# Optimization experiments

Measured on AMD Instinct MI355X. Metric: run time of the kernel, lower is better.

Reference implementation:

```python
import jax, jax.numpy as jnp
import numpy as np

STALENESS_LAMBDA = 0.001
TEMPERATURE = 1.0
TOP_K = 3
EPS = 1e-8


def setup_inputs() -> dict:
    key = jax.random.key(0)
    ks = jax.random.split(key, 6)
    B, D, H, E = 131072, 512, 256, 10
    features = jax.random.normal(ks[0], (B, D), dtype=jnp.float32)
    W_proj = jax.random.normal(ks[1], (D, H), dtype=jnp.float32) * 0.02
    b_proj = jnp.zeros((H,), dtype=jnp.float32)
    expert_emb = jax.random.normal(ks[2], (E, H), dtype=jnp.float32) * 0.01
    expert_features = jax.random.normal(ks[3], (E, D), dtype=jnp.float32)
    trust = jax.random.uniform(ks[4], (E,), dtype=jnp.float32)
    delta_t = jax.random.uniform(ks[5], (E,), dtype=jnp.float32) * 100.0
    return {"features": features, "W_proj": W_proj, "b_proj": b_proj,
            "expert_emb": expert_emb, "expert_features": expert_features,
            "trust": trust, "delta_t": delta_t}


def reference(features, W_proj, b_proj, expert_emb, expert_features, trust, delta_t):
    H = W_proj.shape[1]
    # learned gate: sigmoid(proj(x) . e_j / sqrt(H))  -> (B, E)
    proj = features @ W_proj + b_proj                                  # (B, H)
    gate = jax.nn.sigmoid(jnp.einsum('bh,eh->be', proj, expert_emb)
                          / jnp.sqrt(jnp.float32(H)))
    # cosine similarity S_ij mapped to [0, 1]                          # (B, E)
    fn = features / jnp.maximum(jnp.linalg.norm(features, axis=1, keepdims=True), EPS)
    en = expert_features / jnp.maximum(
        jnp.linalg.norm(expert_features, axis=1, keepdims=True), EPS)
    sim = (jnp.einsum('bd,ed->be', fn, en) + 1.0) * 0.5
    # staleness decay e^{-lambda * dt} and base score T*S*decay
    stale = jnp.exp(-STALENESS_LAMBDA * delta_t)                        # (E,)
    score = gate * (trust * stale)[None, :] * sim                       # (B, E)
    probs = jax.nn.softmax(score / TEMPERATURE, axis=-1)                # (B, E)
    topk_w, topk_idx = jax.lax.top_k(probs, TOP_K)                      # (B, K)
    topk_w = topk_w / jnp.sum(topk_w, axis=-1, keepdims=True)
    return topk_w, topk_idx, probs
```

## Files before the change

kernel.cpp:

```cpp
#include <hip/hip_runtime.h>
#include <stdint.h>
#include <math.h>

#define D_DIM 512
#define H_DIM 256
#define E_NUM 10

typedef float f16v __attribute__((ext_vector_type(16)));
typedef float f2 __attribute__((ext_vector_type(2)));

__global__ __launch_bounds__(256) void pre_wg(const float* __restrict__ Wp,
                                              const float* __restrict__ bp,
                                              const float* __restrict__ emb,
                                              float* __restrict__ pk,
                                              float* __restrict__ bg) {
  int gid = blockIdx.x * 256 + threadIdx.x;
  if (gid < E_NUM * D_DIM) {
    int d = gid / E_NUM;
    int e = gid - d * E_NUM;
    const float* wr = Wp + (size_t)d * H_DIM;
    const float* er = emb + (size_t)e * H_DIM;
    float s0 = 0.f, s1 = 0.f, s2 = 0.f, s3 = 0.f;
#pragma unroll 4
    for (int h = 0; h < H_DIM; h += 4) {
      float4 a = *(const float4*)(wr + h);
      float4 b = *(const float4*)(er + h);
      s0 = fmaf(a.x, b.x, s0); s1 = fmaf(a.y, b.y, s1);
      s2 = fmaf(a.z, b.z, s2); s3 = fmaf(a.w, b.w, s3);
    }
    pk[(size_t)d * 20 + e] = ((s0 + s1) + (s2 + s3)) * 0.0625f;
  } else if (gid < E_NUM * D_DIM + E_NUM) {
    int e = gid - E_NUM * D_DIM;
    const float* er = emb + (size_t)e * H_DIM;
    float s = 0.f;
    for (int h = 0; h < H_DIM; ++h) s = fmaf(bp[h], er[h], s);
    bg[e] = s * 0.0625f;
  }
}

__global__ __launch_bounds__(64) void pre_en(const float* __restrict__ ef,
                                             const float* __restrict__ trust,
                                             const float* __restrict__ dtv,
                                             float* __restrict__ pk,
                                             float* __restrict__ cf) {
  int e = blockIdx.x, l = threadIdx.x;
  const float* row = ef + (size_t)e * D_DIM;
  float s = 0.f;
#pragma unroll
  for (int j = 0; j < D_DIM / 64; ++j) { float v = row[l + 64 * j]; s = fmaf(v, v, s); }
#pragma unroll
  for (int o = 32; o; o >>= 1) s += __shfl_xor(s, o, 64);
  float inv = 1.f / fmaxf(sqrtf(s), 1e-8f);
#pragma unroll
  for (int j = 0; j < D_DIM / 64; ++j) {
    int d = l + 64 * j;
    pk[(size_t)d * 20 + 10 + e] = row[d] * inv;
  }
  if (l == 0) cf[e] = trust[e] * expf(-0.001f * dtv[e]);
}

#define WVx(i) ((i) < 16 ? w0[(i) & 15] : (i) < 32 ? w1[(i) & 15] : \
                (i) < 48 ? w2[(i) & 15] : (i) < 64 ? w3[(i) & 15] : w4[(i) & 15])

__global__ __launch_bounds__(256, 6) void router_main(
    const float* __restrict__ feat, const float* __restrict__ pk,
    const float* __restrict__ cf, const float* __restrict__ bg,
    float* __restrict__ out, int B) {
  __shared__ float red[3 * 64 * 23];
  const int t = threadIdx.x;
  const int l = t & 63;
  const int w = __builtin_amdgcn_readfirstlane(t >> 6);
  const size_t row = (size_t)blockIdx.x * 64 + l;
  const float* gp = feat + row * D_DIM + w * 128;
  const float* wq = pk + (size_t)w * 128 * 20;

  f2 ag[5], as_[5], n2;
#pragma unroll
  for (int i = 0; i < 5; ++i) { ag[i] = f2{0.f, 0.f}; as_[i] = f2{0.f, 0.f}; }
  n2 = f2{0.f, 0.f};

  float4 fvA[4], fvB[4];
#pragma unroll
  for (int j = 0; j < 4; ++j) fvA[j] = *(const float4*)(gp + j * 4);

#pragma unroll
  for (int it = 0; it < 8; ++it) {
    float4* cur = (it & 1) ? fvB : fvA;
    float4* nxt = (it & 1) ? fvA : fvB;
    if (it < 7) {
#pragma unroll
      for (int j = 0; j < 4; ++j) nxt[j] = *(const float4*)(gp + (it + 1) * 16 + j * 4);
    }
#pragma unroll
    for (int sub = 0; sub < 4; ++sub) {
      f16v w0, w1, w2, w3, w4;
      const float* wp = wq + (it * 4 + sub) * 80;
      asm volatile(
          "s_load_dwordx16 %0, %5, 0x0\n"
          "s_load_dwordx16 %1, %5, 0x40\n"
          "s_load_dwordx16 %2, %5, 0x80\n"
          "s_load_dwordx16 %3, %5, 0xc0\n"
          "s_load_dwordx16 %4, %5, 0x100\n"
          "s_waitcnt lgkmcnt(0)"
          : "=&s"(w0), "=&s"(w1), "=&s"(w2), "=&s"(w3), "=&s"(w4)
          : "s"(wp));
      float4 f = cur[sub];
#pragma unroll
      for (int q = 0; q < 4; ++q) {
        const float fq = (q == 0) ? f.x : (q == 1) ? f.y : (q == 2) ? f.z : f.w;
        const f2 fq2 = {fq, fq};
#pragma unroll
        for (int j = 0; j < 5; ++j) {
          const int bgi = q * 20 + 2 * j;
          f2 wg2 = {WVx(bgi), WVx(bgi + 1)};
          ag[j] = __builtin_elementwise_fma(fq2, wg2, ag[j]);
        }
#pragma unroll
        for (int j = 0; j < 5; ++j) {
          const int bsi = q * 20 + 10 + 2 * j;
          f2 ws2 = {WVx(bsi), WVx(bsi + 1)};
          as_[j] = __builtin_elementwise_fma(fq2, ws2, as_[j]);
        }
      }
      f2 p0 = {f.x, f.y}, p1 = {f.z, f.w};
      n2 = __builtin_elementwise_fma(p0, p0, n2);
      n2 = __builtin_elementwise_fma(p1, p1, n2);
    }
  }

  float acc[21];
#pragma unroll
  for (int e = 0; e < E_NUM; ++e) { acc[e] = ag[e >> 1][e & 1]; acc[10 + e] = as_[e >> 1][e & 1]; }
  acc[20] = n2.x + n2.y;

  if (w) {
    float* rp = &red[((w - 1) * 64 + l) * 23];
#pragma unroll
    for (int i = 0; i < 21; ++i) rp[i] = acc[i];
  }
  __syncthreads();
  if (w == 0) {
#pragma unroll
    for (int s = 0; s < 3; ++s) {
      const float* rp = &red[(s * 64 + l) * 23];
#pragma unroll
      for (int i = 0; i < 21; ++i) acc[i] += rp[i];
    }

    const float inv = 1.f / fmaxf(sqrtf(acc[20]), 1e-8f);
    float probs[E_NUM];
    float m = -1e30f;
#pragma unroll
    for (int e = 0; e < E_NUM; ++e) {
      float logit = acc[e] + bg[e];
      float gate = 1.f / (1.f + __expf(-logit));
      float sim = fmaf(acc[10 + e] * inv, 0.5f, 0.5f);
      float sc = gate * cf[e] * sim;
      probs[e] = sc;
      m = fmaxf(m, sc);
    }
    float Z = 0.f;
#pragma unroll
    for (int e = 0; e < E_NUM; ++e) { float pe = __expf(probs[e] - m); probs[e] = pe; Z += pe; }
    const float invZ = 1.f / Z;
#pragma unroll
    for (int e = 0; e < E_NUM; ++e) probs[e] *= invZ;

    int i0 = 0; float b0 = probs[0];
#pragma unroll
    for (int e = 1; e < E_NUM; ++e) if (probs[e] > b0) { b0 = probs[e]; i0 = e; }
    int i1 = -1; float b1 = -1.f;
#pragma unroll
    for (int e = 0; e < E_NUM; ++e) if (e != i0 && probs[e] > b1) { b1 = probs[e]; i1 = e; }
    int i2 = -1; float b2 = -1.f;
#pragma unroll
    for (int e = 0; e < E_NUM; ++e) if (e != i0 && e != i1 && probs[e] > b2) { b2 = probs[e]; i2 = e; }

    const float wnorm = 1.f / (b0 + b1 + b2);
    float* ow = out + row * 3;
    ow[0] = b0 * wnorm; ow[1] = b1 * wnorm; ow[2] = b2 * wnorm;
    float* oi = out + (size_t)B * 3 + row * 3;
    oi[0] = (float)i0; oi[1] = (float)i1; oi[2] = (float)i2;
    float* op = out + (size_t)B * 6 + row * E_NUM;
#pragma unroll
    for (int e = 0; e < E_NUM; ++e) op[e] = probs[e];
  }
}

extern "C" void kernel_launch(void* const* d_in, const int* in_sizes, int n_in,
                              void* d_out, int out_size, void* d_ws, size_t ws_size,
                              hipStream_t stream) {
  const float* feat  = (const float*)d_in[0];
  const float* Wp    = (const float*)d_in[1];
  const float* bp    = (const float*)d_in[2];
  const float* emb   = (const float*)d_in[3];
  const float* ef    = (const float*)d_in[4];
  const float* trust = (const float*)d_in[5];
  const float* dtv   = (const float*)d_in[6];
  float* out = (float*)d_out;

  float* pk = (float*)d_ws;
  float* cf = pk + D_DIM * 20;
  float* bg = cf + E_NUM;

  const int B = in_sizes[0] / D_DIM;

  hipLaunchKernelGGL(pre_wg, dim3((E_NUM * D_DIM + E_NUM + 255) / 256), dim3(256),
                     0, stream, Wp, bp, emb, pk, bg);
  hipLaunchKernelGGL(pre_en, dim3(E_NUM), dim3(64), 0, stream, ef, trust, dtv, pk, cf);
  hipLaunchKernelGGL(router_main, dim3(B / 64), dim3(256), 0, stream,
                     feat, pk, cf, bg, out, B);
}
```

Baseline: 73.68 us.

## Stage feature rows through LDS with async global_load_lds multi-buffer pipeline

Replaces direct per-thread register loads of feature rows with a 4-deep ring of LDS buffers filled by global_load_lds, using XOR-swizzled slots and barrier-synchronised steps. Each block now handles 128 rows, with two half-blocks each covering half of D. The cross-wave reduction is cut to a single partner. The aim is coalesced, asynchronous loads that overlap compute and hide memory latency for this bandwidth-bound kernel, at the cost of a barrier per step, more LDS, and lower occupancy (launch bounds 2 instead of 6).

```diff
diff --git a/kernel.cpp b/kernel.cpp
--- a/kernel.cpp
+++ b/kernel.cpp
@@ -5,6 +5,8 @@
 #define D_DIM 512
 #define H_DIM 256
 #define E_NUM 10
+#define ROWS_PB 128
+#define NSTEP 16
 
 typedef float f16v __attribute__((ext_vector_type(16)));
 typedef float f2 __attribute__((ext_vector_type(2)));
@@ -62,39 +64,43 @@
 #define WVx(i) ((i) < 16 ? w0[(i) & 15] : (i) < 32 ? w1[(i) & 15] : \
                 (i) < 48 ? w2[(i) & 15] : (i) < 64 ? w3[(i) & 15] : w4[(i) & 15])
 
-__global__ __launch_bounds__(256, 6) void router_main(
+__global__ __launch_bounds__(256, 2) void router_main(
     const float* __restrict__ feat, const float* __restrict__ pk,
     const float* __restrict__ cf, const float* __restrict__ bg,
     float* __restrict__ out, int B) {
-  __shared__ float red[3 * 64 * 23];
+  __shared__ float lds[4][ROWS_PB * 32];
   const int t = threadIdx.x;
   const int l = t & 63;
   const int w = __builtin_amdgcn_readfirstlane(t >> 6);
-  const size_t row = (size_t)blockIdx.x * 64 + l;
-  const float* gp = feat + row * D_DIM + w * 128;
-  const float* wq = pk + (size_t)w * 128 * 20;
+  const int h = __builtin_amdgcn_readfirstlane(t >> 7);
+  const int p = t & 127;
+  const size_t r0 = (size_t)blockIdx.x * ROWS_PB;
+
+  const int sr = w * 8 + (l >> 3);
+  const int qg = (l & 7) ^ (l >> 3);
+  const float* gbase = feat + (r0 + sr) * (size_t)D_DIM + ((qg >> 2) * 256 + (qg & 3) * 4);
+  const int ldsbase = w * 8 * 32;
 
   f2 ag[5], as_[5], n2;
 #pragma unroll
   for (int i = 0; i < 5; ++i) { ag[i] = f2{0.f, 0.f}; as_[i] = f2{0.f, 0.f}; }
   n2 = f2{0.f, 0.f};
 
-  float4 fvA[4], fvB[4];
-#pragma unroll
-  for (int j = 0; j < 4; ++j) fvA[j] = *(const float4*)(gp + j * 4);
-
-#pragma unroll
-  for (int it = 0; it < 8; ++it) {
-    float4* cur = (it & 1) ? fvB : fvA;
-    float4* nxt = (it & 1) ? fvA : fvB;
-    if (it < 7) {
-#pragma unroll
-      for (int j = 0; j < 4; ++j) nxt[j] = *(const float4*)(gp + (it + 1) * 16 + j * 4);
-    }
-#pragma unroll
-    for (int sub = 0; sub < 4; ++sub) {
+  auto STAGE = [&](int buf, int c) {
+#pragma unroll
+    for (int j = 0; j < 4; ++j) {
+      __builtin_amdgcn_global_load_lds(
+          (const __attribute__((address_space(1))) uint32_t*)(gbase + (size_t)j * 32 * D_DIM + c * 16),
+          (__attribute__((address_space(3))) uint32_t*)&lds[buf][ldsbase + j * 1024],
+          16, 0, 0);
+    }
+  };
+
+  auto COMPUTE = [&](int buf, int c) {
+#pragma unroll
+    for (int qq = 0; qq < 4; ++qq) {
       f16v w0, w1, w2, w3, w4;
-      const float* wp = wq + (it * 4 + sub) * 80;
+      const float* wp = pk + (size_t)(h * 256 + c * 16 + qq * 4) * 20;
       asm volatile(
           "s_load_dwordx16 %0, %5, 0x0\n"
           "s_load_dwordx16 %1, %5, 0x40\n"
@@ -104,7 +110,8 @@
           "s_waitcnt lgkmcnt(0)"
           : "=&s"(w0), "=&s"(w1), "=&s"(w2), "=&s"(w3), "=&s"(w4)
           : "s"(wp));
-      float4 f = cur[sub];
+      const int slot = ((h << 2) + qq) ^ (p & 7);
+      float4 f = *(const float4*)&lds[buf][p * 32 + slot * 4];
 #pragma unroll
       for (int q = 0; q < 4; ++q) {
         const float fq = (q == 0) ? f.x : (q == 1) ? f.y : (q == 2) ? f.z : f.w;
@@ -126,26 +133,48 @@
       n2 = __builtin_elementwise_fma(p0, p0, n2);
       n2 = __builtin_elementwise_fma(p1, p1, n2);
     }
-  }
+  };
+
+  STAGE(0, 0); STAGE(1, 1); STAGE(2, 2);
+
+#pragma unroll 1
+  for (int c = 0; c < NSTEP - 3; ++c) {
+    asm volatile("s_waitcnt vmcnt(8) lgkmcnt(0)" ::: "memory");
+    __builtin_amdgcn_s_barrier();
+    __builtin_amdgcn_sched_barrier(0);
+    STAGE((c + 3) & 3, c + 3);
+    COMPUTE(c & 3, c);
+  }
+  asm volatile("s_waitcnt vmcnt(8) lgkmcnt(0)" ::: "memory");
+  __builtin_amdgcn_s_barrier();
+  __builtin_amdgcn_sched_barrier(0);
+  COMPUTE(1, 13);
+  asm volatile("s_waitcnt vmcnt(4) lgkmcnt(0)" ::: "memory");
+  __builtin_amdgcn_s_barrier();
+  __builtin_amdgcn_sched_barrier(0);
+  COMPUTE(2, 14);
+  asm volatile("s_waitcnt vmcnt(0) lgkmcnt(0)" ::: "memory");
+  __builtin_amdgcn_s_barrier();
+  __builtin_amdgcn_sched_barrier(0);
+  COMPUTE(3, 15);
 
   float acc[21];
 #pragma unroll
   for (int e = 0; e < E_NUM; ++e) { acc[e] = ag[e >> 1][e & 1]; acc[10 + e] = as_[e >> 1][e & 1]; }
   acc[20] = n2.x + n2.y;
 
-  if (w) {
-    float* rp = &red[((w - 1) * 64 + l) * 23];
+  if (h) {
+    float* rp = &lds[0][p * 23];
 #pragma unroll
     for (int i = 0; i < 21; ++i) rp[i] = acc[i];
   }
-  __syncthreads();
-  if (w == 0) {
-#pragma unroll
-    for (int s = 0; s < 3; ++s) {
-      const float* rp = &red[(s * 64 + l) * 23];
-#pragma unroll
-      for (int i = 0; i < 21; ++i) acc[i] += rp[i];
-    }
+  asm volatile("s_waitcnt lgkmcnt(0)" ::: "memory");
+  __builtin_amdgcn_s_barrier();
+  __builtin_amdgcn_sched_barrier(0);
+  if (h == 0) {
+    const float* rp = &lds[0][p * 23];
+#pragma unroll
+    for (int i = 0; i < 21; ++i) acc[i] += rp[i];
 
     const float inv = 1.f / fmaxf(sqrtf(acc[20]), 1e-8f);
     float probs[E_NUM];
@@ -177,6 +206,7 @@
     for (int e = 0; e < E_NUM; ++e) if (e != i0 && e != i1 && probs[e] > b2) { b2 = probs[e]; i2 = e; }
 
     const float wnorm = 1.f / (b0 + b1 + b2);
+    const size_t row = r0 + p;
     float* ow = out + row * 3;
     ow[0] = b0 * wnorm; ow[1] = b1 * wnorm; ow[2] = b2 * wnorm;
     float* oi = out + (size_t)B * 3 + row * 3;
@@ -208,6 +238,6 @@
   hipLaunchKernelGGL(pre_wg, dim3((E_NUM * D_DIM + E_NUM + 255) / 256), dim3(256),
                      0, stream, Wp, bp, emb, pk, bg);
   hipLaunchKernelGGL(pre_en, dim3(E_NUM), dim3(64), 0, stream, ef, trust, dtv, pk, cf);
-  hipLaunchKernelGGL(router_main, dim3(B / 64), dim3(256), 0, stream,
+  hipLaunchKernelGGL(router_main, dim3(B / ROWS_PB), dim3(256), 0, stream,
                      feat, pk, cf, bg, out, B);
 }
```

Measured after the change: 96.78 us. 31.4% more time.

## Stage feature tiles through LDS with async global_load_lds double buffering

Applied to the files above, without the earlier changes.

Replaces direct per-lane strided float4 global loads of feature rows with coalesced global_load_lds transfers into a swizzled, double-buffered LDS tile per wave, pipelined with explicit vmcnt waits. Each lane then reads its row slice from LDS using an XOR swizzle meant to avoid bank conflicts. The intent is better memory coalescing and overlap of loads with FMA work. LDS use grows to 32KB per block and the occupancy hint drops from 6 to 5 blocks per CU. No barrier separates writing the reduction scratch from the other waves' staging buffers, which adds a risk of overwriting data still in use.

```diff
diff --git a/kernel.cpp b/kernel.cpp
--- a/kernel.cpp
+++ b/kernel.cpp
@@ -62,39 +62,42 @@
 #define WVx(i) ((i) < 16 ? w0[(i) & 15] : (i) < 32 ? w1[(i) & 15] : \
                 (i) < 48 ? w2[(i) & 15] : (i) < 64 ? w3[(i) & 15] : w4[(i) & 15])
 
-__global__ __launch_bounds__(256, 6) void router_main(
+__global__ __launch_bounds__(256, 5) void router_main(
     const float* __restrict__ feat, const float* __restrict__ pk,
     const float* __restrict__ cf, const float* __restrict__ bg,
     float* __restrict__ out, int B) {
-  __shared__ float red[3 * 64 * 23];
+  __shared__ float lds[8192];
   const int t = threadIdx.x;
   const int l = t & 63;
   const int w = __builtin_amdgcn_readfirstlane(t >> 6);
-  const size_t row = (size_t)blockIdx.x * 64 + l;
-  const float* gp = feat + row * D_DIM + w * 128;
-  const float* wq = pk + (size_t)w * 128 * 20;
+  const size_t r0 = (size_t)blockIdx.x * 64;
+  const int wbase = w * 2048;
+
+  const int rpp = l >> 2;
+  const int qsw = (l & 3) ^ (rpp & 3) ^ ((rpp >> 2) & 3);
+  const float* gsrc = feat + (r0 + rpp) * (size_t)D_DIM + w * 128 + qsw * 4;
+  const int csw = ((l & 3) ^ ((l >> 2) & 3)) << 2;
 
   f2 ag[5], as_[5], n2;
 #pragma unroll
   for (int i = 0; i < 5; ++i) { ag[i] = f2{0.f, 0.f}; as_[i] = f2{0.f, 0.f}; }
   n2 = f2{0.f, 0.f};
 
-  float4 fvA[4], fvB[4];
-#pragma unroll
-  for (int j = 0; j < 4; ++j) fvA[j] = *(const float4*)(gp + j * 4);
-
-#pragma unroll
-  for (int it = 0; it < 8; ++it) {
-    float4* cur = (it & 1) ? fvB : fvA;
-    float4* nxt = (it & 1) ? fvA : fvB;
-    if (it < 7) {
-#pragma unroll
-      for (int j = 0; j < 4; ++j) nxt[j] = *(const float4*)(gp + (it + 1) * 16 + j * 4);
-    }
-#pragma unroll
-    for (int sub = 0; sub < 4; ++sub) {
+  auto STAGE = [&](int buf, int c) {
+#pragma unroll
+    for (int j = 0; j < 4; ++j) {
+      __builtin_amdgcn_global_load_lds(
+          (const __attribute__((address_space(1))) uint32_t*)(gsrc + (size_t)j * 16 * D_DIM + c * 16),
+          (__attribute__((address_space(3))) uint32_t*)&lds[wbase + buf * 1024 + j * 256 + (l << 2)],
+          16, 0, 0);
+    }
+  };
+
+  auto COMPUTE = [&](int buf, int c) {
+#pragma unroll
+    for (int qq = 0; qq < 4; ++qq) {
       f16v w0, w1, w2, w3, w4;
-      const float* wp = wq + (it * 4 + sub) * 80;
+      const float* wp = pk + (size_t)(w * 128 + c * 16 + qq * 4) * 20;
       asm volatile(
           "s_load_dwordx16 %0, %5, 0x0\n"
           "s_load_dwordx16 %1, %5, 0x40\n"
@@ -104,7 +107,7 @@
           "s_waitcnt lgkmcnt(0)"
           : "=&s"(w0), "=&s"(w1), "=&s"(w2), "=&s"(w3), "=&s"(w4)
           : "s"(wp));
-      float4 f = cur[sub];
+      float4 f = *(const float4*)&lds[wbase + buf * 1024 + l * 16 + ((qq << 2) ^ csw)];
 #pragma unroll
       for (int q = 0; q < 4; ++q) {
         const float fq = (q == 0) ? f.x : (q == 1) ? f.y : (q == 2) ? f.z : f.w;
@@ -126,7 +129,24 @@
       n2 = __builtin_elementwise_fma(p0, p0, n2);
       n2 = __builtin_elementwise_fma(p1, p1, n2);
     }
-  }
+  };
+
+  STAGE(0, 0); STAGE(1, 1);
+#pragma unroll 1
+  for (int c = 0; c < 6; ++c) {
+    asm volatile("s_waitcnt vmcnt(4)" ::: "memory");
+    __builtin_amdgcn_sched_barrier(0);
+    COMPUTE(c & 1, c);
+    asm volatile("s_waitcnt lgkmcnt(0)" ::: "memory");
+    __builtin_amdgcn_sched_barrier(0);
+    STAGE(c & 1, c + 2);
+  }
+  asm volatile("s_waitcnt vmcnt(4)" ::: "memory");
+  __builtin_amdgcn_sched_barrier(0);
+  COMPUTE(0, 6);
+  asm volatile("s_waitcnt vmcnt(0)" ::: "memory");
+  __builtin_amdgcn_sched_barrier(0);
+  COMPUTE(1, 7);
 
   float acc[21];
 #pragma unroll
@@ -134,15 +154,15 @@
   acc[20] = n2.x + n2.y;
 
   if (w) {
-    float* rp = &red[((w - 1) * 64 + l) * 23];
+    float* rp = &lds[wbase + l * 24];
 #pragma unroll
     for (int i = 0; i < 21; ++i) rp[i] = acc[i];
   }
   __syncthreads();
   if (w == 0) {
 #pragma unroll
-    for (int s = 0; s < 3; ++s) {
-      const float* rp = &red[(s * 64 + l) * 23];
+    for (int s = 1; s < 4; ++s) {
+      const float* rp = &lds[s * 2048 + l * 24];
 #pragma unroll
       for (int i = 0; i < 21; ++i) acc[i] += rp[i];
     }
@@ -177,6 +197,7 @@
     for (int e = 0; e < E_NUM; ++e) if (e != i0 && e != i1 && probs[e] > b2) { b2 = probs[e]; i2 = e; }
 
     const float wnorm = 1.f / (b0 + b1 + b2);
+    const size_t row = r0 + l;
     float* ow = out + row * 3;
     ow[0] = b0 * wnorm; ow[1] = b1 * wnorm; ow[2] = b2 * wnorm;
     float* oi = out + (size_t)B * 3 + row * 3;
```

After: 81.60 us. +10.7%, slower.
